# Optimization experiments

Measured on AMD Instinct MI355X. Metric: run time of the kernel, lower is better.

The kernel has to match this reference:

```python
import jax, jax.numpy as jnp
import numpy as np

D = 1024; H = 8; QLR = 384; KVLR = 256; NOPE = 128; ROPE = 64; VD = 128
E = 8; TOPK = 2; INTER = 512; NSH = 2; B = 2; T = 2048
QKD = NOPE + ROPE  # 192


def _rms(x, w, eps=1e-6):
    return x * jax.lax.rsqrt(jnp.mean(x * x, axis=-1, keepdims=True) + eps) * w


def _rope(x, cos, sin):
    # x: [B,T,h,ROPE]; pairs are consecutive elements (torch view(...,-1,2)).
    x0 = x[..., 0::2]
    x1 = x[..., 1::2]
    c = cos[None, :, None, :]
    s = sin[None, :, None, :]
    y0 = x0 * c - x1 * s
    y1 = x0 * s + x1 * c
    return jnp.stack([y0, y1], axis=-1).reshape(x.shape)


def setup_inputs() -> dict:
    key = jax.random.key(0)
    ks = jax.random.split(key, 12)
    def w(k, shape, scale=0.02):
        return jax.random.normal(k, shape, dtype=jnp.float32) * scale
    inv = 1.0 / (10000.0 ** (jnp.arange(0, ROPE, 2, dtype=jnp.float32) / ROPE))
    ang = jnp.arange(T, dtype=jnp.float32)[:, None] * inv[None, :]  # [T, ROPE//2]
    return {
        "x": jax.random.normal(ks[0], (B, T, D), dtype=jnp.float32),
        "freqs_cos": jnp.cos(ang),
        "freqs_sin": jnp.sin(ang),
        "rmsn1_w": jnp.ones((D,), jnp.float32),
        "rmsn2_w": jnp.ones((D,), jnp.float32),
        "latent_w": w(ks[1], (D, QLR + KVLR + ROPE)),
        "q_norm_w": jnp.ones((QLR,), jnp.float32),
        "q_up_w": w(ks[2], (QLR, H * QKD)),
        "kv_norm_w": jnp.ones((KVLR,), jnp.float32),
        "kv_up_w": w(ks[3], (KVLR, H * (NOPE + VD))),
        "c_proj_w": w(ks[4], (D, D)),
        "gate_w": w(ks[5], (D, E)),
        "sh_w1": w(ks[6], (D, INTER * NSH)),
        "sh_w2": w(ks[7], (INTER * NSH, D)),
        "sh_w3": w(ks[8], (D, INTER * NSH)),
        "e_w1": w(ks[9], (E, D, INTER)),
        "e_w2": w(ks[10], (E, INTER, D)),
        "e_w3": w(ks[11], (E, D, INTER)),
    }


def reference(x, freqs_cos, freqs_sin, rmsn1_w, rmsn2_w, latent_w, q_norm_w,
              q_up_w, kv_norm_w, kv_up_w, c_proj_w, gate_w, sh_w1, sh_w2,
              sh_w3, e_w1, e_w2, e_w3):
    Bx, Tx, _ = x.shape
    # ---- MLA attention ----
    h = _rms(x, rmsn1_w)
    lat = h @ latent_w
    q_l, kv_l, k_r = jnp.split(lat, [QLR, QLR + KVLR], axis=-1)
    q = (_rms(q_l, q_norm_w) @ q_up_w).reshape(Bx, Tx, H, QKD)
    q_n, q_r = q[..., :NOPE], q[..., NOPE:]
    q_r = _rope(q_r, freqs_cos, freqs_sin)
    q = jnp.concatenate([q_n, q_r], axis=-1)  # [B,T,H,QKD]
    kv = (_rms(kv_l, kv_norm_w) @ kv_up_w).reshape(Bx, Tx, H, NOPE + VD)
    k_n, v = kv[..., :NOPE], kv[..., NOPE:]
    k_r = _rope(k_r[:, :, None, :], freqs_cos, freqs_sin)
    k_r = jnp.broadcast_to(k_r, (Bx, Tx, H, ROPE))
    k = jnp.concatenate([k_n, k_r], axis=-1)
    scale = 1.0 / jnp.sqrt(jnp.float32(QKD))
    scores = jnp.einsum('bqhd,bkhd->bhqk', q, k) * scale
    causal = jnp.tril(jnp.ones((Tx, Tx), dtype=bool))
    scores = jnp.where(causal, scores, jnp.finfo(scores.dtype).min)
    attn = jax.nn.softmax(scores, axis=-1)
    y = jnp.einsum('bhqk,bkhd->bqhd', attn, v).reshape(Bx, Tx, D)
    x = x + y @ c_proj_w
    # ---- DeepSeekMoE ----
    h2 = _rms(x, rmsn2_w).reshape(-1, D)  # [N, D]
    y_sh = (jax.nn.silu(h2 @ sh_w1) * (h2 @ sh_w3)) @ sh_w2
    scores_g = jax.nn.softmax(h2 @ gate_w, axis=-1)  # [N, E]
    w_top, idx = jax.lax.top_k(scores_g, TOPK)  # weights == gathered original scores
    # combine weights per expert (route_scale = 1.0)
    cw = jnp.sum(jax.nn.one_hot(idx, E, dtype=h2.dtype) * w_top[..., None], axis=1)  # [N, E]
    h1 = jnp.einsum('nd,edi->eni', h2, e_w1)
    h3 = jnp.einsum('nd,edi->eni', h2, e_w3)
    out_e = jnp.einsum('eni,eid->end', jax.nn.silu(h1) * h3, e_w2)  # [E, N, D]
    y_moe = y_sh + jnp.einsum('end,ne->nd', out_e, cw)
    return x + y_moe.reshape(Bx, Tx, D)
```

## Files before the change

### kernel.cpp

```cpp
#include <hip/hip_runtime.h>
#include <hip/hip_bf16.h>
#include <math.h>

#define D_ 1024
#define H_ 8
#define QLR_ 384
#define KVLR_ 256
#define NOPE_ 128
#define ROPE_ 64
#define VD_ 128
#define E_ 8
#define INTER_ 512
#define B_ 2
#define T_ 2048
#define QKD_ 192
#define NTOK (B_*T_)
#define LSTR 4608
#define MAXMB 72

typedef __attribute__((ext_vector_type(8))) short short8;
typedef __attribute__((ext_vector_type(4))) float f32x4;
typedef __attribute__((ext_vector_type(4))) unsigned short us4;

__device__ __forceinline__ unsigned short f2bf(float f) {
  union { float f; unsigned u; } v; v.f = f;
  return (unsigned short)((v.u + 0x7FFFu + ((v.u >> 16) & 1u)) >> 16);
}
__device__ __forceinline__ float bf2f(unsigned short h) {
  union { unsigned u; float f; } v; v.u = ((unsigned)h) << 16;
  return v.f;
}

#define GLD16(SRC, DST) __builtin_amdgcn_global_load_lds( \
    (__attribute__((address_space(1))) void*)(SRC), \
    (__attribute__((address_space(3))) void*)(DST), 16, 0, 0)

#define DPPF(v, ctrl) __int_as_float(__builtin_amdgcn_update_dpp(0, __float_as_int(v), ctrl, 0xF, 0xF, true))
__device__ __forceinline__ float dppmax16(float v) {
  v = fmaxf(v, DPPF(v, 0xB1));
  v = fmaxf(v, DPPF(v, 0x4E));
  v = fmaxf(v, DPPF(v, 0x124));
  v = fmaxf(v, DPPF(v, 0x128));
  return v;
}
__device__ __forceinline__ float dppsum16(float v) {
  v += DPPF(v, 0xB1);
  v += DPPF(v, 0x4E);
  v += DPPF(v, 0x124);
  v += DPPF(v, 0x128);
  return v;
}

__global__ __launch_bounds__(256) void transpose_f32_bf16(
    const float* __restrict__ in, unsigned short* __restrict__ out,
    int R, int C, size_t inBS, size_t outBS) {
  __shared__ float tile[32][33];
  const float* inp = in + (size_t)blockIdx.z * inBS;
  unsigned short* outp = out + (size_t)blockIdx.z * outBS;
  int c0 = blockIdx.x * 32, r0 = blockIdx.y * 32;
  int tx = threadIdx.x & 31, ty = threadIdx.x >> 5;
  #pragma unroll
  for (int i = 0; i < 4; ++i) {
    int rr = ty + i * 8;
    tile[rr][tx] = inp[(size_t)(r0 + rr) * C + c0 + tx];
  }
  __syncthreads();
  #pragma unroll
  for (int i = 0; i < 4; ++i) {
    int rr = ty + i * 8;
    outp[(size_t)(c0 + rr) * R + r0 + tx] = f2bf(tile[tx][rr]);
  }
}

__global__ __launch_bounds__(256) void transpose_pair(
    const float* __restrict__ in1, const float* __restrict__ in3,
    unsigned short* __restrict__ out, int K, int C1, size_t inBS, size_t outBS) {
  __shared__ float tile[32][33];
  int z = blockIdx.z; int bat = z >> 1; int f = (z & 1) * 16;
  const float* src = ((z & 1) ? in3 : in1) + (size_t)bat * inBS;
  unsigned short* o = out + (size_t)bat * outBS;
  int c0 = blockIdx.x * 32, r0 = blockIdx.y * 32;
  int tx = threadIdx.x & 31, ty = threadIdx.x >> 5;
  #pragma unroll
  for (int i = 0; i < 4; ++i) {
    int rr = ty + i * 8;
    tile[rr][tx] = src[(size_t)(r0 + rr) * C1 + c0 + tx];
  }
  __syncthreads();
  #pragma unroll
  for (int i = 0; i < 4; ++i) {
    int cc = ty + i * 8;
    int c = c0 + cc;
    int n = ((c >> 4) << 5) + (c & 15) + f;
    o[(size_t)n * K + r0 + tx] = f2bf(tile[tx][cc]);
  }
}

template<typename TI>
__global__ __launch_bounds__(256) void rms_to_bf16(
    const TI* __restrict__ src, int stride, int off, const float* __restrict__ w,
    unsigned short* __restrict__ out, int Dd, int outStride) {
  int row = blockIdx.x;
  const TI* xr = src + (size_t)row * stride + off;
  float ss = 0.f;
  for (int i = threadIdx.x; i < Dd; i += 256) {
    float v;
    if constexpr (sizeof(TI) == 2) v = bf2f((unsigned short)xr[i]); else v = (float)xr[i];
    ss += v * v;
  }
  for (int o = 1; o < 64; o <<= 1) ss += __shfl_xor(ss, o);
  __shared__ float red[4];
  if ((threadIdx.x & 63) == 0) red[threadIdx.x >> 6] = ss;
  __syncthreads();
  float tot = red[0] + red[1] + red[2] + red[3];
  float inv = 1.f / sqrtf(tot / Dd + 1e-6f);
  for (int i = threadIdx.x; i < Dd; i += 256) {
    float v;
    if constexpr (sizeof(TI) == 2) v = bf2f((unsigned short)xr[i]); else v = (float)xr[i];
    out[(size_t)row * outStride + i] = f2bf(v * inv * w[i]);
  }
}

__global__ __launch_bounds__(256) void lat_post(
    const unsigned short* __restrict__ lat, const float* __restrict__ qw,
    const float* __restrict__ kw, const float* __restrict__ fc, const float* __restrict__ fs,
    unsigned short* __restrict__ qn, unsigned short* __restrict__ kvn,
    unsigned short* __restrict__ kr) {
  int row = blockIdx.x, tid = threadIdx.x;
  int lane = tid & 63, wv = tid >> 6;
  const unsigned short* lr = lat + (size_t)row * 768;
  float s1 = 0.f, s2 = 0.f;
  for (int i = tid; i < QLR_; i += 256) { float v = bf2f(lr[i]); s1 += v * v; }
  { float v = bf2f(lr[QLR_ + tid]); s2 = v * v; }
  for (int o = 1; o < 64; o <<= 1) { s1 += __shfl_xor(s1, o); s2 += __shfl_xor(s2, o); }
  __shared__ float red[8];
  if (lane == 0) { red[wv] = s1; red[4 + wv] = s2; }
  __syncthreads();
  float inv1 = 1.f / sqrtf((red[0] + red[1] + red[2] + red[3]) / QLR_ + 1e-6f);
  float inv2 = 1.f / sqrtf((red[4] + red[5] + red[6] + red[7]) / KVLR_ + 1e-6f);
  for (int i = tid; i < QLR_; i += 256)
    qn[(size_t)row * QLR_ + i] = f2bf(bf2f(lr[i]) * inv1 * qw[i]);
  kvn[(size_t)row * KVLR_ + tid] = f2bf(bf2f(lr[QLR_ + tid]) * inv2 * kw[tid]);
  if (tid < 32) {
    int t = row & (T_ - 1);
    float c = fc[t * 32 + tid], s = fs[t * 32 + tid];
    float x0 = bf2f(lr[640 + 2 * tid]), x1 = bf2f(lr[640 + 2 * tid + 1]);
    kr[(size_t)row * ROPE_ + 2 * tid]     = f2bf(x0 * c - x1 * s);
    kr[(size_t)row * ROPE_ + 2 * tid + 1] = f2bf(x0 * s + x1 * c);
  }
}

template<int MODE>
__global__ __launch_bounds__(256) void gemm_bf16(
    const unsigned short* __restrict__ A, const unsigned short* __restrict__ Bt,
    void* __restrict__ Cv, int M, int N, int K,
    const float* __restrict__ addv, unsigned short* __restrict__ vtg) {
  __shared__ __align__(16) unsigned short As[128 * 32];
  __shared__ __align__(16) unsigned short Bs[128 * 32];
  const int tid = threadIdx.x;
  const int lane = tid & 63, wave = tid >> 6;
  const int wm = wave >> 1, wn = wave & 1;
  const int bm = blockIdx.y * 128, bn = blockIdx.x * 128;
  const int r = lane & 15, g = lane >> 4;

  f32x4 acc[4][4];
  #pragma unroll
  for (int i = 0; i < 4; ++i)
    #pragma unroll
    for (int j = 0; j < 4; ++j) acc[i][j] = (f32x4)0.f;

  const int rl0 = wave * 16 + (lane >> 2);
  const int rl1 = rl0 + 64;
  const int kc = (lane & 3) * 8;
  char* AsB = (char*)As; char* BsB = (char*)Bs;

  for (int k0 = 0; k0 < K; k0 += 32) {
    GLD16(A + (size_t)(bm + rl0) * K + k0 + kc, AsB + wave * 1024);
    GLD16(A + (size_t)(bm + rl1) * K + k0 + kc, AsB + (wave + 4) * 1024);
    GLD16(Bt + (size_t)(bn + rl0) * K + k0 + kc, BsB + wave * 1024);
    GLD16(Bt + (size_t)(bn + rl1) * K + k0 + kc, BsB + (wave + 4) * 1024);
    __syncthreads();
    short8 af[4], bfr[4];
    #pragma unroll
    for (int mi = 0; mi < 4; ++mi)
      af[mi] = *(const short8*)(As + (wm * 64 + mi * 16 + r) * 32 + g * 8);
    #pragma unroll
    for (int nj = 0; nj < 4; ++nj)
      bfr[nj] = *(const short8*)(Bs + (wn * 64 + nj * 16 + r) * 32 + g * 8);
    #pragma unroll
    for (int mi = 0; mi < 4; ++mi)
      #pragma unroll
      for (int nj = 0; nj < 4; ++nj)
        acc[mi][nj] = __builtin_amdgcn_mfma_f32_16x16x32_bf16(af[mi], bfr[nj], acc[mi][nj], 0, 0, 0);
    __syncthreads();
  }

  if (MODE == 5) {
    unsigned short* C = (unsigned short*)Cv;
    const int colbase = bn + wn * 64;
    const int b = bm >> 11;
    const int hh = colbase >> 8;
    if ((colbase & 255) < 128) {
      #pragma unroll
      for (int mi = 0; mi < 4; ++mi)
        #pragma unroll
        for (int reg = 0; reg < 4; ++reg) {
          int mrow = bm + wm * 64 + mi * 16 + g * 4 + reg;
          size_t bas = (size_t)mrow * N + colbase + r;
          #pragma unroll
          for (int nj = 0; nj < 4; ++nj) C[bas + nj * 16] = f2bf(acc[mi][nj][reg]);
        }
    } else {
      const int tl0 = (bm & 2047) + wm * 64 + g * 4;
      const int d0 = (colbase & 255) - 128 + r;
      #pragma unroll
      for (int mi = 0; mi < 4; ++mi)
        #pragma unroll
        for (int nj = 0; nj < 4; ++nj) {
          int d = d0 + nj * 16;
          us4 pk;
          #pragma unroll
          for (int reg = 0; reg < 4; ++reg) pk[reg] = f2bf(acc[mi][nj][reg]);
          *(us4*)(vtg + ((size_t)((b * 8 + hh) * 128 + d)) * 2048 + tl0 + mi * 16) = pk;
        }
    }
    return;
  }

  const int orow0 = wm * 64 + g * 4;
  const int ocol0 = bn + wn * 64 + r;
  #pragma unroll
  for (int mi = 0; mi < 4; ++mi) {
    #pragma unroll
    for (int reg = 0; reg < 4; ++reg) {
      int mrow = bm + orow0 + mi * 16 + reg;
      if (MODE == 4) {
        unsigned short* C = (unsigned short*)Cv;
        size_t bas2 = (size_t)mrow * (N >> 1) + ((bn + wn * 64) >> 1) + r;
        #pragma unroll
        for (int p = 0; p < 2; ++p) {
          float a = acc[mi][2 * p][reg], b3 = acc[mi][2 * p + 1][reg];
          C[bas2 + p * 16] = f2bf((a / (1.f + __expf(-a))) * b3);
        }
      } else {
        size_t bas = (size_t)mrow * N + ocol0;
        if (MODE == 0) {
          unsigned short* C = (unsigned short*)Cv;
          #pragma unroll
          for (int nj = 0; nj < 4; ++nj) C[bas + nj * 16] = f2bf(acc[mi][nj][reg]);
        } else if (MODE == 1) {
          float* C = (float*)Cv;
          #pragma unroll
          for (int nj = 0; nj < 4; ++nj) C[bas + nj * 16] = acc[mi][nj][reg] + addv[bas + nj * 16];
        } else {
          float* C = (float*)Cv;
          #pragma unroll
          for (int nj = 0; nj < 4; ++nj) C[bas + nj * 16] += acc[mi][nj][reg];
        }
      }
    }
  }
}

__global__ __launch_bounds__(256) void gemm_moe13(
    const unsigned short* __restrict__ A, const unsigned short* __restrict__ W,
    unsigned short* __restrict__ Cb,
    const int* __restrict__ lists, const int* __restrict__ map, const int* __restrict__ sbase) {
  int mb = map[blockIdx.y];
  if (mb < 0) return;
  const int e = mb >> 16, ib = mb & 0xFFFF;
  __shared__ __align__(16) unsigned short As[128 * 32];
  __shared__ __align__(16) unsigned short Bs[128 * 32];
  const int tid = threadIdx.x, lane = tid & 63, wave = tid >> 6;
  const int wm = wave >> 1, wn = wave & 1;
  const int bn = blockIdx.x * 128;
  const int r = lane & 15, g = lane >> 4;

  f32x4 acc[4][4];
  #pragma unroll
  for (int i = 0; i < 4; ++i)
    #pragma unroll
    for (int j = 0; j < 4; ++j) acc[i][j] = (f32x4)0.f;

  const int rl0 = wave * 16 + (lane >> 2), rl1 = rl0 + 64;
  const int kc = (lane & 3) * 8;
  int t0 = lists[e * LSTR + ib * 128 + rl0]; if (t0 < 0) t0 = 0;
  int t1 = lists[e * LSTR + ib * 128 + rl1]; if (t1 < 0) t1 = 0;
  const unsigned short* Wb = W + (size_t)e * 1024 * 1024;
  char* AsB = (char*)As; char* BsB = (char*)Bs;

  for (int k0 = 0; k0 < 1024; k0 += 32) {
    GLD16(A + (size_t)t0 * 1024 + k0 + kc, AsB + wave * 1024);
    GLD16(A + (size_t)t1 * 1024 + k0 + kc, AsB + (wave + 4) * 1024);
    GLD16(Wb + (size_t)(bn + rl0) * 1024 + k0 + kc, BsB + wave * 1024);
    GLD16(Wb + (size_t)(bn + rl1) * 1024 + k0 + kc, BsB + (wave + 4) * 1024);
    __syncthreads();
    short8 af[4], bfr[4];
    #pragma unroll
    for (int mi = 0; mi < 4; ++mi)
      af[mi] = *(const short8*)(As + (wm * 64 + mi * 16 + r) * 32 + g * 8);
    #pragma unroll
    for (int nj = 0; nj < 4; ++nj)
      bfr[nj] = *(const short8*)(Bs + (wn * 64 + nj * 16 + r) * 32 + g * 8);
    #pragma unroll
    for (int mi = 0; mi < 4; ++mi)
      #pragma unroll
      for (int nj = 0; nj < 4; ++nj)
        acc[mi][nj] = __builtin_amdgcn_mfma_f32_16x16x32_bf16(af[mi], bfr[nj], acc[mi][nj], 0, 0, 0);
    __syncthreads();
  }
  const int sb = sbase[e] + ib * 128;
  const int hc = ((bn + wn * 64) >> 1) + r;
  #pragma unroll
  for (int mi = 0; mi < 4; ++mi)
    #pragma unroll
    for (int reg = 0; reg < 4; ++reg) {
      int srow = sb + wm * 64 + mi * 16 + g * 4 + reg;
      #pragma unroll
      for (int p = 0; p < 2; ++p) {
        float a = acc[mi][2 * p][reg], b3 = acc[mi][2 * p + 1][reg];
        Cb[(size_t)srow * 512 + hc + p * 16] = f2bf((a / (1.f + __expf(-a))) * b3);
      }
    }
}

__global__ __launch_bounds__(256) void gemm_moe2(
    const unsigned short* __restrict__ Am, const unsigned short* __restrict__ W,
    float* __restrict__ out,
    const int* __restrict__ lists, const int* __restrict__ map, const int* __restrict__ sbase,
    const float* __restrict__ cw) {
  int mb = map[blockIdx.y];
  if (mb < 0) return;
  const int e = mb >> 16, ib = mb & 0xFFFF;
  __shared__ __align__(16) unsigned short As[128 * 32];
  __shared__ __align__(16) unsigned short Bs[128 * 32];
  const int tid = threadIdx.x, lane = tid & 63, wave = tid >> 6;
  const int wm = wave >> 1, wn = wave & 1;
  const int bn = blockIdx.x * 128;
  const int r = lane & 15, g = lane >> 4;

  f32x4 acc[4][4];
  #pragma unroll
  for (int i = 0; i < 4; ++i)
    #pragma unroll
    for (int j = 0; j < 4; ++j) acc[i][j] = (f32x4)0.f;

  const int rl0 = wave * 16 + (lane >> 2), rl1 = rl0 + 64;
  const int kc = (lane & 3) * 8;
  const int sb = sbase[e] + ib * 128;
  const unsigned short* Wb = W + (size_t)e * 512 * 1024;
  char* AsB = (char*)As; char* BsB = (char*)Bs;

  for (int k0 = 0; k0 < 512; k0 += 32) {
    GLD16(Am + (size_t)(sb + rl0) * 512 + k0 + kc, AsB + wave * 1024);
    GLD16(Am + (size_t)(sb + rl1) * 512 + k0 + kc, AsB + (wave + 4) * 1024);
    GLD16(Wb + (size_t)(bn + rl0) * 512 + k0 + kc, BsB + wave * 1024);
    GLD16(Wb + (size_t)(bn + rl1) * 512 + k0 + kc, BsB + (wave + 4) * 1024);
    __syncthreads();
    short8 af[4], bfr[4];
    #pragma unroll
    for (int mi = 0; mi < 4; ++mi)
      af[mi] = *(const short8*)(As + (wm * 64 + mi * 16 + r) * 32 + g * 8);
    #pragma unroll
    for (int nj = 0; nj < 4; ++nj)
      bfr[nj] = *(const short8*)(Bs + (wn * 64 + nj * 16 + r) * 32 + g * 8);
    #pragma unroll
    for (int mi = 0; mi < 4; ++mi)
      #pragma unroll
      for (int nj = 0; nj < 4; ++nj)
        acc[mi][nj] = __builtin_amdgcn_mfma_f32_16x16x32_bf16(af[mi], bfr[nj], acc[mi][nj], 0, 0, 0);
    __syncthreads();
  }
  const int ocol0 = bn + wn * 64 + r;
  #pragma unroll
  for (int mi = 0; mi < 4; ++mi)
    #pragma unroll
    for (int reg = 0; reg < 4; ++reg) {
      int orow = wm * 64 + mi * 16 + g * 4 + reg;
      int tok = lists[e * LSTR + ib * 128 + orow];
      if (tok >= 0) {
        float wt = cw[(size_t)tok * E_ + e];
        #pragma unroll
        for (int nj = 0; nj < 4; ++nj)
          atomicAdd(out + (size_t)tok * 1024 + ocol0 + nj * 16, acc[mi][nj][reg] * wt);
      }
    }
}

#define AQ 64
#define AK 32
#define VP 40
__global__ __launch_bounds__(256) void attn_mfma(
    const unsigned short* __restrict__ q,
    const unsigned short* __restrict__ kv,
    const unsigned short* __restrict__ kr,
    const unsigned short* __restrict__ vt,
    const float* __restrict__ fcos, const float* __restrict__ fsin,
    unsigned short* __restrict__ y) {
  __shared__ __align__(16) unsigned short Qs[AQ * 192];
  __shared__ __align__(16) unsigned short Ks[AK * 192];
  __shared__ __align__(16) unsigned short Vl[128 * VP];
  __shared__ __align__(16) unsigned short Ps[4 * 16 * VP];
  const int tid = threadIdx.x, lane = tid & 63, wave = tid >> 6;
  const int r = lane & 15, g = lane >> 4;
  const int bh = blockIdx.y, b = bh >> 3, h = bh & 7;
  const int qt = gridDim.x - 1 - blockIdx.x;
  const int q0 = qt * AQ;
  const size_t bT = (size_t)b * T_;
  const unsigned short* vbase = vt + (size_t)bh * 128 * T_;
  char* QsB = (char*)Qs; char* KsB = (char*)Ks;

  #pragma unroll
  for (int it = 0; it < 6; ++it) {
    int c = tid + it * 256;
    int row = c / 24, c8 = c % 24;
    short8 v = *(const short8*)(q + ((bT + q0 + row) * H_ + h) * 192 + c8 * 8);
    if (c8 >= 16) {
      int t = q0 + row;
      int ib = (c8 - 16) * 4;
      #pragma unroll
      for (int p = 0; p < 4; ++p) {
        float cc = fcos[t * 32 + ib + p], sn = fsin[t * 32 + ib + p];
        float x0 = bf2f((unsigned short)v[2 * p]), x1 = bf2f((unsigned short)v[2 * p + 1]);
        v[2 * p]     = (short)f2bf(x0 * cc - x1 * sn);
        v[2 * p + 1] = (short)f2bf(x0 * sn + x1 * cc);
      }
    }
    *(short8*)(QsB + ((row * 384 + c8 * 16) ^ ((row & 7) << 4))) = v;
  }

  float m_i[4], l_i[4];
  f32x4 o[8];
  #pragma unroll
  for (int i = 0; i < 4; ++i) { m_i[i] = -1e30f; l_i[i] = 0.f; }
  #pragma unroll
  for (int cb = 0; cb < 8; ++cb) o[cb] = (f32x4)0.f;

  const float scale2 = 0.07216878364870322f * 1.44269504088896f;
  const int ntiles = q0 / AK + 2;

  short8 kreg[3], vreg[2];
  int krow[3], kcol[3];
  #pragma unroll
  for (int it = 0; it < 3; ++it) {
    int c = tid + it * 256;
    krow[it] = c / 24; kcol[it] = c % 24;
    kreg[it] = (kcol[it] < 16)
      ? *(const short8*)(kv + ((bT + krow[it]) * H_ + h) * 256 + kcol[it] * 8)
      : *(const short8*)(kr + (bT + krow[it]) * 64 + (kcol[it] - 16) * 8);
  }
  #pragma unroll
  for (int it = 0; it < 2; ++it) {
    int x = tid + it * 256;
    vreg[it] = *(const short8*)(vbase + (size_t)(x >> 2) * T_ + (x & 3) * 8);
  }

  for (int kt = 0; kt < ntiles; ++kt) {
    __syncthreads();
    #pragma unroll
    for (int it = 0; it < 3; ++it)
      *(short8*)(KsB + ((krow[it] * 384 + kcol[it] * 16) ^ ((krow[it] & 7) << 4))) = kreg[it];
    #pragma unroll
    for (int it = 0; it < 2; ++it) {
      int x = tid + it * 256;
      *(short8*)(Vl + (x >> 2) * VP + (x & 3) * 8) = vreg[it];
    }
    __syncthreads();

    if (kt + 1 < ntiles) {
      int k1 = (kt + 1) * AK;
      #pragma unroll
      for (int it = 0; it < 3; ++it)
        kreg[it] = (kcol[it] < 16)
          ? *(const short8*)(kv + ((bT + k1 + krow[it]) * H_ + h) * 256 + kcol[it] * 8)
          : *(const short8*)(kr + (bT + k1 + krow[it]) * 64 + (kcol[it] - 16) * 8);
      #pragma unroll
      for (int it = 0; it < 2; ++it) {
        int x = tid + it * 256;
        vreg[it] = *(const short8*)(vbase + (size_t)(x >> 2) * T_ + k1 + (x & 3) * 8);
      }
    }

    const int k0 = kt * AK;
    f32x4 sf0 = (f32x4)0.f, sf1 = (f32x4)0.f;
    {
      int qrow = wave * 16 + r;
      int qsw = (qrow & 7) << 4, ksw = (r & 7) << 4;
      __builtin_amdgcn_s_setprio(1);
      #pragma unroll
      for (int kk = 0; kk < 6; ++kk) {
        short8 aq = *(const short8*)(QsB + ((qrow * 384 + kk * 64 + g * 16) ^ qsw));
        short8 b0 = *(const short8*)(KsB + ((r * 384 + kk * 64 + g * 16) ^ ksw));
        short8 b1 = *(const short8*)(KsB + (((16 + r) * 384 + kk * 64 + g * 16) ^ ksw));
        sf0 = __builtin_amdgcn_mfma_f32_16x16x32_bf16(aq, b0, sf0, 0, 0, 0);
        sf1 = __builtin_amdgcn_mfma_f32_16x16x32_bf16(aq, b1, sf1, 0, 0, 0);
      }
      __builtin_amdgcn_s_setprio(0);
    }
    float fac[4];
    bool needs = false;
    #pragma unroll
    for (int reg = 0; reg < 4; ++reg) {
      float s0 = sf0[reg] * scale2;
      float s1 = sf1[reg] * scale2;
      int qp = q0 + wave * 16 + g * 4 + reg;
      if (k0 + r > qp) s0 = -1e30f;
      if (k0 + 16 + r > qp) s1 = -1e30f;
      float mt = dppmax16(fmaxf(s0, s1));
      float fc = 1.f, mn = m_i[reg];
      if (mt > mn + 8.f) {
        mn = mt; fc = exp2f(m_i[reg] - mn); m_i[reg] = mn; needs = true;
      }
      float e0 = exp2f(s0 - mn), e1 = exp2f(s1 - mn);
      float rs = dppsum16(e0 + e1);
      l_i[reg] = l_i[reg] * fc + rs;
      fac[reg] = fc;
      __hip_bfloat162 pk = __float22bfloat162_rn(float2{e0, e1});
      unsigned u = *(unsigned*)&pk;
      int prow = g * 4 + reg;
      Ps[wave * 16 * VP + prow * VP + r] = (unsigned short)u;
      Ps[wave * 16 * VP + prow * VP + 16 + r] = (unsigned short)(u >> 16);
    }
    if (__any(needs)) {
      #pragma unroll
      for (int cb = 0; cb < 8; ++cb)
        #pragma unroll
        for (int reg = 0; reg < 4; ++reg) o[cb][reg] *= fac[reg];
    }
    short8 pa = *(const short8*)(Ps + wave * 16 * VP + r * VP + g * 8);
    __builtin_amdgcn_s_setprio(1);
    #pragma unroll
    for (int cb = 0; cb < 8; ++cb) {
      short8 vb = *(const short8*)(Vl + (cb * 16 + r) * VP + g * 8);
      o[cb] = __builtin_amdgcn_mfma_f32_16x16x32_bf16(pa, vb, o[cb], 0, 0, 0);
    }
    __builtin_amdgcn_s_setprio(0);
  }

  #pragma unroll
  for (int reg = 0; reg < 4; ++reg) {
    float inv = 1.f / l_i[reg];
    int nrow = q0 + wave * 16 + g * 4 + reg;
    size_t bas = (bT + nrow) * (size_t)D_ + h * VD_;
    #pragma unroll
    for (int cb = 0; cb < 8; ++cb)
      y[bas + cb * 16 + r] = f2bf(o[cb][reg] * inv);
  }
}

__global__ __launch_bounds__(256) void rms2_gate(
    const float* __restrict__ xo, const float* __restrict__ rw, const float* __restrict__ gw,
    unsigned short* __restrict__ h2b, float* __restrict__ cw) {
  int row = blockIdx.x, tid = threadIdx.x;
  int lane = tid & 63, wv = tid >> 6;
  const float* xr = xo + (size_t)row * D_;
  float v[4]; float ss = 0.f;
  #pragma unroll
  for (int j = 0; j < 4; ++j) { v[j] = xr[tid + j * 256]; ss += v[j] * v[j]; }
  for (int o = 1; o < 64; o <<= 1) ss += __shfl_xor(ss, o);
  __shared__ float red[4];
  if (lane == 0) red[wv] = ss;
  __syncthreads();
  float inv = 1.f / sqrtf((red[0] + red[1] + red[2] + red[3]) / D_ + 1e-6f);
  float a[E_] = {0, 0, 0, 0, 0, 0, 0, 0};
  #pragma unroll
  for (int j = 0; j < 4; ++j) {
    int i = tid + j * 256;
    float hv = v[j] * inv * rw[i];
    h2b[(size_t)row * D_ + i] = f2bf(hv);
    const float* wr = gw + (size_t)i * E_;
    #pragma unroll
    for (int e = 0; e < E_; ++e) a[e] += hv * wr[e];
  }
  #pragma unroll
  for (int e = 0; e < E_; ++e) {
    float t = a[e];
    for (int o = 1; o < 64; o <<= 1) t += __shfl_xor(t, o);
    a[e] = t;
  }
  __shared__ float ga[4][E_];
  if (lane == 0)
    #pragma unroll
    for (int e = 0; e < E_; ++e) ga[wv][e] = a[e];
  __syncthreads();
  if (tid == 0) {
    float lg[E_];
    #pragma unroll
    for (int e = 0; e < E_; ++e) lg[e] = ga[0][e] + ga[1][e] + ga[2][e] + ga[3][e];
    float mx = lg[0];
    #pragma unroll
    for (int e = 1; e < E_; ++e) mx = fmaxf(mx, lg[e]);
    float sum = 0.f; float p[E_];
    #pragma unroll
    for (int e = 0; e < E_; ++e) { p[e] = __expf(lg[e] - mx); sum += p[e]; }
    float is = 1.f / sum;
    int i1 = 0; float b1 = p[0];
    #pragma unroll
    for (int e = 1; e < E_; ++e) if (p[e] > b1) { b1 = p[e]; i1 = e; }
    int i2 = -1; float b2 = -1.f;
    #pragma unroll
    for (int e = 0; e < E_; ++e) if (e != i1 && p[e] > b2) { b2 = p[e]; i2 = e; }
    #pragma unroll
    for (int e = 0; e < E_; ++e)
      cw[(size_t)row * E_ + e] = (e == i1) ? b1 * is : (e == i2 ? b2 * is : 0.f);
  }
}

__global__ __launch_bounds__(256) void moe_build(const float* __restrict__ cw,
                                                 int* __restrict__ lists, int* __restrict__ counts) {
  int e = blockIdx.x, tid = threadIdx.x;
  int lane = tid & 63, wv = tid >> 6;
  __shared__ int wsum[4];
  __shared__ int base;
  if (tid == 0) base = 0;
  __syncthreads();
  for (int c0 = 0; c0 < NTOK; c0 += 256) {
    int tok = c0 + tid;
    bool f = cw[(size_t)tok * E_ + e] > 0.f;
    unsigned long long m = __ballot(f);
    int pos = __popcll(m & ((1ull << lane) - 1ull));
    if (lane == 0) wsum[wv] = __popcll(m);
    __syncthreads();
    int woff = base;
    #pragma unroll
    for (int w = 0; w < 4; ++w) if (w < wv) woff += wsum[w];
    if (f) lists[e * LSTR + woff + pos] = tok;
    __syncthreads();
    if (tid == 0) base += wsum[0] + wsum[1] + wsum[2] + wsum[3];
    __syncthreads();
  }
  int cnt = base;
  int padded = (cnt + 127) & ~127;
  for (int i2 = cnt + tid; i2 < padded; i2 += 256) lists[e * LSTR + i2] = -1;
  if (tid == 0) { counts[e] = cnt; counts[8 + e] = padded >> 7; }
}

__global__ void moe_finalize(const int* __restrict__ counts, int* __restrict__ map,
                             int* __restrict__ sbase) {
  if (threadIdx.x == 0 && blockIdx.x == 0) {
    int cum = 0;
    for (int e = 0; e < E_; ++e) {
      sbase[e] = cum * 128;
      int nb = counts[8 + e];
      for (int i = 0; i < nb; ++i) map[cum + i] = (e << 16) | i;
      cum += nb;
    }
    for (; cum < MAXMB; ++cum) map[cum] = -1;
  }
}

extern "C" void kernel_launch(void* const* d_in, const int* in_sizes, int n_in,
                              void* d_out, int out_size, void* d_ws, size_t ws_size,
                              hipStream_t stream) {
  const float* x        = (const float*)d_in[0];
  const float* fcos     = (const float*)d_in[1];
  const float* fsin     = (const float*)d_in[2];
  const float* rmsn1_w  = (const float*)d_in[3];
  const float* rmsn2_w  = (const float*)d_in[4];
  const float* latent_w = (const float*)d_in[5];
  const float* q_norm_w = (const float*)d_in[6];
  const float* q_up_w   = (const float*)d_in[7];
  const float* kv_norm_w= (const float*)d_in[8];
  const float* kv_up_w  = (const float*)d_in[9];
  const float* c_proj_w = (const float*)d_in[10];
  const float* gate_w   = (const float*)d_in[11];
  const float* sh_w1    = (const float*)d_in[12];
  const float* sh_w2    = (const float*)d_in[13];
  const float* sh_w3    = (const float*)d_in[14];
  const float* e_w1     = (const float*)d_in[15];
  const float* e_w2     = (const float*)d_in[16];
  const float* e_w3     = (const float*)d_in[17];
  float* out = (float*)d_out;

  char* base = (char*)d_ws;
  size_t off = 0;
  auto take = [&](size_t bytes) { char* p = base + off; off += (bytes + 255) & ~(size_t)255; return p; };
  unsigned short* Wlat  = (unsigned short*)take((size_t)768 * 1024 * 2);
  unsigned short* Wqup  = (unsigned short*)take((size_t)1536 * 384 * 2);
  unsigned short* Wkv   = (unsigned short*)take((size_t)2048 * 256 * 2);
  unsigned short* Wcp   = (unsigned short*)take((size_t)1024 * 1024 * 2);
  unsigned short* Wsh13 = (unsigned short*)take((size_t)2048 * 1024 * 2);
  unsigned short* Wsh2  = (unsigned short*)take((size_t)1024 * 1024 * 2);
  unsigned short* Wew13 = (unsigned short*)take((size_t)8 * 1024 * 1024 * 2);
  unsigned short* Wew2  = (unsigned short*)take((size_t)8 * 1024 * 512 * 2);
  float* cw             = (float*)take((size_t)NTOK * E_ * 4);
  int* lists            = (int*)take((size_t)E_ * LSTR * 4);
  int* counts           = (int*)take(64 * 4);
  int* map              = (int*)take(MAXMB * 4);
  int* sbase            = (int*)take(E_ * 4);
  unsigned short* Vtg   = (unsigned short*)take((size_t)16 * 128 * T_ * 2);
  unsigned short* kr    = (unsigned short*)take((size_t)NTOK * 64 * 2);

  size_t actStart = off;
  size_t aoff = actStart;
  auto takeA = [&](size_t bytes) { char* p = base + aoff; aoff += (bytes + 255) & ~(size_t)255; return p; };
  unsigned short* h_bf = (unsigned short*)takeA((size_t)NTOK * 1024 * 2);
  unsigned short* lat  = (unsigned short*)takeA((size_t)NTOK * 768 * 2);
  unsigned short* qn   = (unsigned short*)takeA((size_t)NTOK * 384 * 2);
  unsigned short* kvn  = (unsigned short*)takeA((size_t)NTOK * 256 * 2);
  unsigned short* qq   = (unsigned short*)takeA((size_t)NTOK * 1536 * 2);
  unsigned short* kvb  = (unsigned short*)takeA((size_t)NTOK * 2048 * 2);
  unsigned short* y    = (unsigned short*)takeA((size_t)NTOK * 1024 * 2);

  size_t coff = actStart;
  auto takeC = [&](size_t bytes) { char* p = base + coff; coff += (bytes + 255) & ~(size_t)255; return p; };
  unsigned short* h2b  = (unsigned short*)takeC((size_t)NTOK * 1024 * 2);
  unsigned short* t1m  = (unsigned short*)takeC((size_t)NTOK * 1024 * 2);
  unsigned short* ehm  = (unsigned short*)takeC((size_t)9216 * 512 * 2);

  dim3 blk(256);

  transpose_f32_bf16<<<dim3(22, 32, 1), blk, 0, stream>>>(latent_w, Wlat, 1024, 704, 0, 0);
  transpose_f32_bf16<<<dim3(48, 12, 1), blk, 0, stream>>>(q_up_w, Wqup, 384, 1536, 0, 0);
  transpose_f32_bf16<<<dim3(64, 8, 1), blk, 0, stream>>>(kv_up_w, Wkv, 256, 2048, 0, 0);
  transpose_f32_bf16<<<dim3(32, 32, 1), blk, 0, stream>>>(c_proj_w, Wcp, 1024, 1024, 0, 0);
  transpose_f32_bf16<<<dim3(32, 32, 1), blk, 0, stream>>>(sh_w2, Wsh2, 1024, 1024, 0, 0);
  transpose_pair<<<dim3(32, 32, 2), blk, 0, stream>>>(sh_w1, sh_w3, Wsh13, 1024, 1024, 0, 0);
  transpose_pair<<<dim3(16, 32, 16), blk, 0, stream>>>(e_w1, e_w3, Wew13, 1024, 512,
      (size_t)1024 * 512, (size_t)1024 * 1024);
  transpose_f32_bf16<<<dim3(32, 16, 8), blk, 0, stream>>>(e_w2, Wew2, 512, 1024,
      (size_t)512 * 1024, (size_t)1024 * 512);

  rms_to_bf16<float><<<NTOK, blk, 0, stream>>>(x, D_, 0, rmsn1_w, h_bf, D_, D_);
  gemm_bf16<0><<<dim3(6, 32), blk, 0, stream>>>(h_bf, Wlat, lat, NTOK, 768, 1024, nullptr, nullptr);
  lat_post<<<NTOK, blk, 0, stream>>>(lat, q_norm_w, kv_norm_w, fcos, fsin, qn, kvn, kr);
  gemm_bf16<0><<<dim3(12, 32), blk, 0, stream>>>(qn, Wqup, qq, NTOK, 1536, 384, nullptr, nullptr);
  gemm_bf16<5><<<dim3(16, 32), blk, 0, stream>>>(kvn, Wkv, kvb, NTOK, 2048, 256, nullptr, Vtg);
  attn_mfma<<<dim3(T_ / AQ, B_ * H_), blk, 0, stream>>>(qq, kvb, kr, Vtg, fcos, fsin, y);
  gemm_bf16<1><<<dim3(8, 32), blk, 0, stream>>>(y, Wcp, out, NTOK, 1024, 1024, x, nullptr);
  rms2_gate<<<NTOK, blk, 0, stream>>>(out, rmsn2_w, gate_w, h2b, cw);
  moe_build<<<E_, blk, 0, stream>>>(cw, lists, counts);
  moe_finalize<<<1, 64, 0, stream>>>(counts, map, sbase);
  gemm_bf16<4><<<dim3(16, 32), blk, 0, stream>>>(h2b, Wsh13, t1m, NTOK, 2048, 1024, nullptr, nullptr);
  gemm_bf16<2><<<dim3(8, 32), blk, 0, stream>>>(t1m, Wsh2, out, NTOK, 1024, 1024, nullptr, nullptr);
  gemm_moe13<<<dim3(8, MAXMB), blk, 0, stream>>>(h2b, Wew13, ehm, lists, map, sbase);
  gemm_moe2<<<dim3(8, MAXMB), blk, 0, stream>>>(ehm, Wew2, out, lists, map, sbase, cw);
}
```

Before: 410.3 us.

## Split causal attention key range across two blocks and add combine kernel

Result: slower. 446.4 us (+8.8%).

```diff
diff --git a/kernel.cpp b/kernel.cpp
--- a/kernel.cpp
+++ b/kernel.cpp
@@ -396,9 +396,9 @@
     const unsigned short* __restrict__ kr,
     const unsigned short* __restrict__ vt,
     const float* __restrict__ fcos, const float* __restrict__ fsin,
-    unsigned short* __restrict__ y) {
-  __shared__ __align__(16) unsigned short Qs[AQ * 192];
-  __shared__ __align__(16) unsigned short Ks[AK * 192];
+    unsigned short* __restrict__ po,
+    float* __restrict__ pml) {
+  __shared__ __align__(16) unsigned short Ks[24 * 32 * 8];
   __shared__ __align__(16) unsigned short Vl[128 * VP];
   __shared__ __align__(16) unsigned short Ps[4 * 16 * VP];
   const int tid = threadIdx.x, lane = tid & 63, wave = tid >> 6;
@@ -406,27 +406,29 @@
   const int bh = blockIdx.y, b = bh >> 3, h = bh & 7;
   const int qt = gridDim.x - 1 - blockIdx.x;
   const int q0 = qt * AQ;
+  const int half = blockIdx.z;
+  const int hnt = qt + 1;
+  const int kb = half * hnt, ke = kb + hnt;
   const size_t bT = (size_t)b * T_;
   const unsigned short* vbase = vt + (size_t)bh * 128 * T_;
-  char* QsB = (char*)Qs; char* KsB = (char*)Ks;
-
-  #pragma unroll
-  for (int it = 0; it < 6; ++it) {
-    int c = tid + it * 256;
-    int row = c / 24, c8 = c % 24;
-    short8 v = *(const short8*)(q + ((bT + q0 + row) * H_ + h) * 192 + c8 * 8);
-    if (c8 >= 16) {
-      int t = q0 + row;
-      int ib = (c8 - 16) * 4;
+
+  short8 qf[6];
+  const int qrow = q0 + wave * 16 + r;
+  {
+    const unsigned short* qb = q + ((bT + qrow) * H_ + h) * 192;
+    #pragma unroll
+    for (int kk = 0; kk < 6; ++kk) qf[kk] = *(const short8*)(qb + kk * 32 + g * 8);
+    #pragma unroll
+    for (int kk = 4; kk < 6; ++kk) {
+      int i0 = (kk - 4) * 16 + g * 4;
       #pragma unroll
       for (int p = 0; p < 4; ++p) {
-        float cc = fcos[t * 32 + ib + p], sn = fsin[t * 32 + ib + p];
-        float x0 = bf2f((unsigned short)v[2 * p]), x1 = bf2f((unsigned short)v[2 * p + 1]);
-        v[2 * p]     = (short)f2bf(x0 * cc - x1 * sn);
-        v[2 * p + 1] = (short)f2bf(x0 * sn + x1 * cc);
+        float cc = fcos[qrow * 32 + i0 + p], sn = fsin[qrow * 32 + i0 + p];
+        float x0 = bf2f((unsigned short)qf[kk][2 * p]), x1 = bf2f((unsigned short)qf[kk][2 * p + 1]);
+        qf[kk][2 * p]     = (short)f2bf(x0 * cc - x1 * sn);
+        qf[kk][2 * p + 1] = (short)f2bf(x0 * sn + x1 * cc);
       }
     }
-    *(short8*)(QsB + ((row * 384 + c8 * 16) ^ ((row & 7) << 4))) = v;
   }
 
   float m_i[4], l_i[4];
@@ -437,7 +439,6 @@
   for (int cb = 0; cb < 8; ++cb) o[cb] = (f32x4)0.f;
 
   const float scale2 = 0.07216878364870322f * 1.44269504088896f;
-  const int ntiles = q0 / AK + 2;
 
   short8 kreg[3], vreg[2];
   int krow[3], kcol[3];
@@ -446,20 +447,20 @@
     int c = tid + it * 256;
     krow[it] = c / 24; kcol[it] = c % 24;
     kreg[it] = (kcol[it] < 16)
-      ? *(const short8*)(kv + ((bT + krow[it]) * H_ + h) * 256 + kcol[it] * 8)
-      : *(const short8*)(kr + (bT + krow[it]) * 64 + (kcol[it] - 16) * 8);
+      ? *(const short8*)(kv + ((bT + kb * AK + krow[it]) * H_ + h) * 256 + kcol[it] * 8)
+      : *(const short8*)(kr + (bT + kb * AK + krow[it]) * 64 + (kcol[it] - 16) * 8);
   }
   #pragma unroll
   for (int it = 0; it < 2; ++it) {
     int x = tid + it * 256;
-    vreg[it] = *(const short8*)(vbase + (size_t)(x >> 2) * T_ + (x & 3) * 8);
-  }
-
-  for (int kt = 0; kt < ntiles; ++kt) {
+    vreg[it] = *(const short8*)(vbase + (size_t)(x >> 2) * T_ + kb * AK + (x & 3) * 8);
+  }
+
+  for (int kt = kb; kt < ke; ++kt) {
     __syncthreads();
     #pragma unroll
     for (int it = 0; it < 3; ++it)
-      *(short8*)(KsB + ((krow[it] * 384 + kcol[it] * 16) ^ ((krow[it] & 7) << 4))) = kreg[it];
+      *(short8*)(Ks + (kcol[it] * 32 + krow[it]) * 8) = kreg[it];
     #pragma unroll
     for (int it = 0; it < 2; ++it) {
       int x = tid + it * 256;
@@ -467,7 +468,7 @@
     }
     __syncthreads();
 
-    if (kt + 1 < ntiles) {
+    if (kt + 1 < ke) {
       int k1 = (kt + 1) * AK;
       #pragma unroll
       for (int it = 0; it < 3; ++it)
@@ -483,20 +484,16 @@
 
     const int k0 = kt * AK;
     f32x4 sf0 = (f32x4)0.f, sf1 = (f32x4)0.f;
-    {
-      int qrow = wave * 16 + r;
-      int qsw = (qrow & 7) << 4, ksw = (r & 7) << 4;
-      __builtin_amdgcn_s_setprio(1);
-      #pragma unroll
-      for (int kk = 0; kk < 6; ++kk) {
-        short8 aq = *(const short8*)(QsB + ((qrow * 384 + kk * 64 + g * 16) ^ qsw));
-        short8 b0 = *(const short8*)(KsB + ((r * 384 + kk * 64 + g * 16) ^ ksw));
-        short8 b1 = *(const short8*)(KsB + (((16 + r) * 384 + kk * 64 + g * 16) ^ ksw));
-        sf0 = __builtin_amdgcn_mfma_f32_16x16x32_bf16(aq, b0, sf0, 0, 0, 0);
-        sf1 = __builtin_amdgcn_mfma_f32_16x16x32_bf16(aq, b1, sf1, 0, 0, 0);
-      }
-      __builtin_amdgcn_s_setprio(0);
-    }
+    __builtin_amdgcn_s_setprio(1);
+    #pragma unroll
+    for (int kk = 0; kk < 6; ++kk) {
+      short8 b0 = *(const short8*)(Ks + (((kk * 4 + g) * 32) + r) * 8);
+      short8 b1 = *(const short8*)(Ks + (((kk * 4 + g) * 32) + 16 + r) * 8);
+      sf0 = __builtin_amdgcn_mfma_f32_16x16x32_bf16(qf[kk], b0, sf0, 0, 0, 0);
+      sf1 = __builtin_amdgcn_mfma_f32_16x16x32_bf16(qf[kk], b1, sf1, 0, 0, 0);
+    }
+    __builtin_amdgcn_s_setprio(0);
+
     float fac[4];
     bool needs = false;
     #pragma unroll
@@ -537,14 +534,44 @@
     __builtin_amdgcn_s_setprio(0);
   }
 
+  const int slab = (bh * 32 + qt) * 2 + half;
+  unsigned short* pob = po + (size_t)slab * 8192;
+  float* pmlb = pml + (size_t)slab * 128;
   #pragma unroll
   for (int reg = 0; reg < 4; ++reg) {
-    float inv = 1.f / l_i[reg];
-    int nrow = q0 + wave * 16 + g * 4 + reg;
-    size_t bas = (bT + nrow) * (size_t)D_ + h * VD_;
+    int row = wave * 16 + g * 4 + reg;
+    if (r == 0) { pmlb[row * 2] = m_i[reg]; pmlb[row * 2 + 1] = l_i[reg]; }
     #pragma unroll
     for (int cb = 0; cb < 8; ++cb)
-      y[bas + cb * 16 + r] = f2bf(o[cb][reg] * inv);
+      pob[row * 128 + cb * 16 + r] = f2bf(o[cb][reg]);
+  }
+}
+
+__global__ __launch_bounds__(256) void attn_combine(
+    const unsigned short* __restrict__ po, const float* __restrict__ pml,
+    unsigned short* __restrict__ y) {
+  const int qt = blockIdx.x, bh = blockIdx.y, b = bh >> 3, h = bh & 7;
+  const int s0 = (bh * 32 + qt) * 2, s1 = s0 + 1;
+  const int row = threadIdx.x >> 2;
+  const int qp = threadIdx.x & 3;
+  float m0 = pml[(size_t)s0 * 128 + row * 2], l0 = pml[(size_t)s0 * 128 + row * 2 + 1];
+  float m1 = pml[(size_t)s1 * 128 + row * 2], l1 = pml[(size_t)s1 * 128 + row * 2 + 1];
+  float m = fmaxf(m0, m1);
+  float e0 = exp2f(m0 - m), e1 = exp2f(m1 - m);
+  float inv = 1.f / (l0 * e0 + l1 * e1);
+  e0 *= inv; e1 *= inv;
+  const unsigned short* o0 = po + (size_t)s0 * 8192 + row * 128 + qp * 32;
+  const unsigned short* o1 = po + (size_t)s1 * 8192 + row * 128 + qp * 32;
+  unsigned short* yb = y + ((size_t)(b * T_ + qt * 64 + row)) * 1024 + h * 128 + qp * 32;
+  #pragma unroll
+  for (int v = 0; v < 4; ++v) {
+    short8 a = *(const short8*)(o0 + v * 8);
+    short8 c = *(const short8*)(o1 + v * 8);
+    short8 w;
+    #pragma unroll
+    for (int j = 0; j < 8; ++j)
+      w[j] = (short)f2bf(bf2f((unsigned short)a[j]) * e0 + bf2f((unsigned short)c[j]) * e1);
+    *(short8*)(yb + v * 8) = w;
   }
 }
 
@@ -690,6 +717,7 @@
   int* sbase            = (int*)take(E_ * 4);
   unsigned short* Vtg   = (unsigned short*)take((size_t)16 * 128 * T_ * 2);
   unsigned short* kr    = (unsigned short*)take((size_t)NTOK * 64 * 2);
+  float* pml            = (float*)take((size_t)1024 * 128 * 4);
 
   size_t actStart = off;
   size_t aoff = actStart;
@@ -702,6 +730,8 @@
   unsigned short* kvb  = (unsigned short*)takeA((size_t)NTOK * 2048 * 2);
   unsigned short* y    = (unsigned short*)takeA((size_t)NTOK * 1024 * 2);
 
+  unsigned short* po   = (unsigned short*)(base + actStart);
+
   size_t coff = actStart;
   auto takeC = [&](size_t bytes) { char* p = base + coff; coff += (bytes + 255) & ~(size_t)255; return p; };
   unsigned short* h2b  = (unsigned short*)takeC((size_t)NTOK * 1024 * 2);
@@ -726,7 +756,8 @@
   lat_post<<<NTOK, blk, 0, stream>>>(lat, q_norm_w, kv_norm_w, fcos, fsin, qn, kvn, kr);
   gemm_bf16<0><<<dim3(12, 32), blk, 0, stream>>>(qn, Wqup, qq, NTOK, 1536, 384, nullptr, nullptr);
   gemm_bf16<5><<<dim3(16, 32), blk, 0, stream>>>(kvn, Wkv, kvb, NTOK, 2048, 256, nullptr, Vtg);
-  attn_mfma<<<dim3(T_ / AQ, B_ * H_), blk, 0, stream>>>(qq, kvb, kr, Vtg, fcos, fsin, y);
+  attn_mfma<<<dim3(T_ / AQ, B_ * H_, 2), blk, 0, stream>>>(qq, kvb, kr, Vtg, fcos, fsin, po, pml);
+  attn_combine<<<dim3(T_ / AQ, B_ * H_), blk, 0, stream>>>(po, pml, y);
   gemm_bf16<1><<<dim3(8, 32), blk, 0, stream>>>(y, Wcp, out, NTOK, 1024, 1024, x, nullptr);
   rms2_gate<<<NTOK, blk, 0, stream>>>(out, rmsn2_w, gate_w, h2b, cw);
   moe_build<<<E_, blk, 0, stream>>>(cw, lists, counts);
```
